# Optimization experiments

Hardware: AMD Instinct MI355X
Metric: run time of the kernel (lower is better)

## Reference

```python
import jax, jax.numpy as jnp
import numpy as np

B, S = 32, 128
VIN, VOUT = 32000, 32000
D, H, A = 256, 512, 128


def setup_inputs() -> dict:
    key = jax.random.key(0)
    ks = jax.random.split(key, 14)
    p = lambda k, sh: 0.02 * jax.random.normal(k, sh, jnp.float32)
    return {
        "tokens": jax.random.randint(ks[0], (B, S), 0, VIN + 1, dtype=jnp.int32),
        "emb": p(ks[1], (VIN + 1, D)),
        # forward encoder GRU (keras reset_after=True: separate input/recurrent bias)
        "Wx_f": p(ks[2], (D, 3 * H)), "Wh_f": p(ks[3], (H, 3 * H)),
        "bi_f": jnp.zeros((3 * H,), jnp.float32), "br_f": jnp.zeros((3 * H,), jnp.float32),
        # backward encoder GRU
        "Wx_b": p(ks[4], (D, 3 * H)), "Wh_b": p(ks[5], (H, 3 * H)),
        "bi_b": jnp.zeros((3 * H,), jnp.float32), "br_b": jnp.zeros((3 * H,), jnp.float32),
        # additive attention
        "W_a": p(ks[6], (A, H)), "U_a": p(ks[7], (A, 2 * H)), "V_a": p(ks[8], (1, A)),
        # decoder GRUCell (input = [enc_t, ctx] -> 4H)
        "Wx_d": p(ks[9], (4 * H, 3 * H)), "Wh_d": p(ks[10], (H, 3 * H)),
        "bi_d": jnp.zeros((3 * H,), jnp.float32), "br_d": jnp.zeros((3 * H,), jnp.float32),
        # output projection
        "Wo": p(ks[11], (H, VOUT + 1)), "bo": jnp.zeros((VOUT + 1,), jnp.float32),
    }


def _gru_step(h, x, Wx, Wh, bi, br):
    # keras GRU, gate order [z, r, h], reset_after=True
    gx = x @ Wx + bi
    gh = h @ Wh + br
    xz, xr, xh = jnp.split(gx, 3, axis=-1)
    hz, hr, hh = jnp.split(gh, 3, axis=-1)
    z = jax.nn.sigmoid(xz + hz)
    r = jax.nn.sigmoid(xr + hr)
    hc = jnp.tanh(xh + r * hh)
    return z * h + (1.0 - z) * hc


def _run_gru(xs, h0, Wx, Wh, bi, br):
    def f(h, x):
        hn = _gru_step(h, x, Wx, Wh, bi, br)
        return hn, hn
    return jax.lax.scan(f, h0, xs)  # xs: [S,B,D]


def _forward(tokens, emb, Wx_f, Wh_f, bi_f, br_f, Wx_b, Wh_b, bi_b, br_b,
             W_a, U_a, V_a, Wx_d, Wh_d, bi_d, br_d, Wo, bo):
    x = emb[tokens]                      # [B,S,D]
    xs = jnp.transpose(x, (1, 0, 2))     # [S,B,D]
    h0 = jnp.zeros((tokens.shape[0], H), x.dtype)
    _, ys_f = _run_gru(xs, h0, Wx_f, Wh_f, bi_f, br_f)
    hb, ys_b_rev = _run_gru(xs[::-1], h0, Wx_b, Wh_b, bi_b, br_b)
    enc_t = jnp.concatenate([ys_f, ys_b_rev[::-1]], axis=-1)  # [S,B,2H]
    enc = jnp.transpose(enc_t, (1, 0, 2))                     # [B,S,2H]
    U_enc = jnp.einsum('bsd,ad->bsa', enc, U_a)               # hoisted: loop-invariant
    v = V_a[0]                                                # [A]

    def dec_step(h, x_t):
        wh = h @ W_a.T                                        # [B,A]
        score = jnp.einsum('bsa,a->bs', jnp.tanh(wh[:, None, :] + U_enc), v)
        alpha = jax.nn.softmax(score, axis=-1)
        ctx = jnp.einsum('bs,bsd->bd', alpha, enc)            # [B,2H]
        din = jnp.concatenate([x_t, ctx], axis=-1)            # [B,4H]
        hn = _gru_step(h, din, Wx_d, Wh_d, bi_d, br_d)
        return hn, hn

    _, dec_seq = jax.lax.scan(dec_step, hb, enc_t)            # [S,B,H]
    dec = jnp.transpose(dec_seq, (1, 0, 2))                   # [B,S,H]
    logits = dec @ Wo + bo                                    # [B,S,VOUT+1]
    return jax.nn.softmax(logits, axis=-1)


def reference(tokens, emb, Wx_f, Wh_f, bi_f, br_f, Wx_b, Wh_b, bi_b, br_b,
              W_a, U_a, V_a, Wx_d, Wh_d, bi_d, br_d, Wo, bo):
    return _forward(tokens, emb, Wx_f, Wh_f, bi_f, br_f, Wx_b, Wh_b, bi_b, br_b,
                    W_a, U_a, V_a, Wx_d, Wh_d, bi_d, br_d, Wo, bo)
```

## Files before the change

kernel.cpp:

```cpp
#include <hip/hip_runtime.h>
#include <stdint.h>

typedef unsigned int u32;
typedef unsigned long long u64;
typedef __attribute__((ext_vector_type(8))) short bf16x8;
typedef __attribute__((ext_vector_type(4))) float f32x4;
typedef __attribute__((ext_vector_type(4))) int i32x4;
typedef __attribute__((ext_vector_type(2))) int i32x2;

#define DEV static __device__ __forceinline__

DEV short f2bf(float f){ u32 u=__float_as_uint(f); return (short)((u + 0x7fffu + ((u>>16)&1u))>>16); }
DEV float bf2f(short s){ return __uint_as_float(((u32)(unsigned short)s)<<16); }
DEV float sig_p(float x){ return 1.f/(1.f+expf(-x)); }
DEV float tanh_fast(float x){ float e=__expf(2.f*x); return 1.f-2.f/(e+1.f); }

DEV u32  cohl4(const u32* p){ return __hip_atomic_load(p, __ATOMIC_RELAXED, __HIP_MEMORY_SCOPE_AGENT); }
DEV void cohs4(u32* p, u32 v){ __hip_atomic_store(p, v, __ATOMIC_RELAXED, __HIP_MEMORY_SCOPE_AGENT); }
DEV void cohs8(void* p, u64 v){ __hip_atomic_store((u64*)p, v, __ATOMIC_RELAXED, __HIP_MEMORY_SCOPE_AGENT); }
DEV void pollnz(const u32* s){ while (cohl4(s) == 0u) {} }


__global__ void cvt1d(const float* __restrict__ in, short* __restrict__ out, int n){
  int i = blockIdx.x*256 + threadIdx.x;
  if (i < n) out[i] = f2bf(in[i]);
}

__global__ void tconv(const float* __restrict__ in, short* __restrict__ out, int R, int C, int Cpad){
  __shared__ float t[32][33];
  int tx = threadIdx.x, ty = threadIdx.y;
  int c0 = blockIdx.x*32, r0 = blockIdx.y*32;
#pragma unroll
  for (int j=0;j<4;++j){
    int r = r0 + ty + 8*j, c = c0 + tx;
    t[ty+8*j][tx] = (c < C) ? in[(size_t)r*C + c] : 0.f;
  }
  __syncthreads();
#pragma unroll
  for (int j=0;j<4;++j){
    int oc = c0 + ty + 8*j;
    out[(size_t)oc*R + r0 + tx] = f2bf(t[tx][ty+8*j]);
  }
}

__global__ void btrans(const short* __restrict__ in, short* __restrict__ out, int Dd){
  __shared__ short t[32][33];
  int tx = threadIdx.x, ty = threadIdx.y;
  int d0 = blockIdx.x*32, s = blockIdx.y;
#pragma unroll
  for (int j=0;j<4;++j)
    t[ty+8*j][tx] = in[((size_t)s*Dd + d0 + ty + 8*j)*32 + tx];
  __syncthreads();
#pragma unroll
  for (int j=0;j<4;++j)
    out[((size_t)(s*32 + ty + 8*j))*Dd + d0 + tx] = t[tx][ty+8*j];
}

__global__ void etrans(const short* __restrict__ in, short* __restrict__ out){
  __shared__ short t[128][33];
  int c = blockIdx.x, tid = threadIdx.x;
#pragma unroll
  for (int i=0;i<16;++i){
    int idx = tid + i*256;
    t[idx>>5][idx&31] = in[((size_t)(idx>>5)*1536 + c)*32 + (idx&31)];
  }
  __syncthreads();
#pragma unroll
  for (int i=0;i<16;++i){
    int idx = tid + i*256;
    out[((size_t)(idx>>7)*1536 + c)*128 + (idx&127)] = t[idx&127][idx>>7];
  }
}

__global__ void embed_k(const int* __restrict__ tok, const float* __restrict__ emb, short* __restrict__ X){
  int row = blockIdx.x;
  int s = row >> 5, b = row & 31;
  int tv = tok[b*128 + s];
  X[(size_t)row*256 + threadIdx.x] = f2bf(emb[(size_t)tv*256 + threadIdx.x]);
}

template<int MODE>
__global__ __launch_bounds__(256) void gemm_k(
  const short* __restrict__ A, const short* __restrict__ BT,
  const float* __restrict__ bias, void* __restrict__ outp,
  float* __restrict__ psum, int Nreal, int K, int Ntot)
{
  const int m0 = blockIdx.y * 128, n0 = blockIdx.x * 128;
  const int tid = threadIdx.x, l = tid & 63, wv = tid >> 6;
  const int wm = wv >> 1, wn = wv & 1;
  __shared__ __align__(16) short As[128*64];
  __shared__ __align__(16) short Bs[128*64];
  f32x4 acc[4][4];
#pragma unroll
  for (int i=0;i<4;++i)
#pragma unroll
    for (int j=0;j<4;++j) acc[i][j] = (f32x4){0.f,0.f,0.f,0.f};

  const int nkb = K >> 6;
  for (int kb=0; kb<nkb; ++kb){
#pragma unroll
    for (int i=0;i<4;++i){
      int si = tid + i*256;
      int row = si >> 3, seg = si & 7;
      u32 off = (u32)(row*128 + seg*16) ^ (u32)((row&7)<<4);
      *(i32x4*)((char*)As + off) = *(const i32x4*)(A + (size_t)(m0+row)*K + kb*64 + seg*8);
      *(i32x4*)((char*)Bs + off) = *(const i32x4*)(BT + (size_t)(n0+row)*K + kb*64 + seg*8);
    }
    __syncthreads();
#pragma unroll
    for (int kt=0; kt<2; ++kt){
      bf16x8 af[4], bfv[4];
      int seg = kt*4 + (l>>4);
#pragma unroll
      for (int f=0; f<4; ++f){
        int ra = wm*64 + f*16 + (l&15);
        af[f]  = *(const bf16x8*)((char*)As + (((u32)(ra*128 + seg*16)) ^ ((u32)(ra&7)<<4)));
        int rb = wn*64 + f*16 + (l&15);
        bfv[f] = *(const bf16x8*)((char*)Bs + (((u32)(rb*128 + seg*16)) ^ ((u32)(rb&7)<<4)));
      }
#pragma unroll
      for (int mf=0; mf<4; ++mf)
#pragma unroll
        for (int nf=0; nf<4; ++nf)
          acc[mf][nf] = __builtin_amdgcn_mfma_f32_16x16x32_bf16(af[mf], bfv[nf], acc[mf][nf], 0,0,0);
    }
    __syncthreads();
  }

  if (MODE == 1){
    short* oT = (short*)outp;
#pragma unroll
    for (int mf=0; mf<4; ++mf){
      int r0 = m0 + wm*64 + mf*16 + ((l>>4)<<2);
      int s = r0 >> 5, b0 = r0 & 31;
#pragma unroll
      for (int nf=0; nf<4; ++nf){
        int col = n0 + wn*64 + nf*16 + (l&15);
        float bv = bias ? bias[col] : 0.f;
        short tmp[4];
#pragma unroll
        for (int j=0;j<4;++j) tmp[j] = f2bf(acc[mf][nf][j] + bv);
        *(i32x2*)(oT + ((size_t)s*Ntot + col)*32 + b0) = *(i32x2*)tmp;
      }
    }
  } else if (MODE == 3){
    short* o = (short*)outp;
#pragma unroll
    for (int mf=0; mf<4; ++mf){
      int r0 = m0 + wm*64 + mf*16 + ((l>>4)<<2);
#pragma unroll
      for (int nf=0; nf<4; ++nf){
        int col = n0 + wn*64 + nf*16 + (l&15);
        if (col < Nreal){
          float bv = bias ? bias[col] : 0.f;
#pragma unroll
          for (int j=0;j<4;++j) o[(size_t)(r0+j)*Nreal + col] = f2bf(acc[mf][nf][j] + bv);
        }
      }
    }
  } else {
    float* o = (float*)outp;
    int ncb = gridDim.x;
    float rs[4][4];
#pragma unroll
    for (int i=0;i<4;++i)
#pragma unroll
      for (int j=0;j<4;++j) rs[i][j]=0.f;
#pragma unroll
    for (int mf=0; mf<4; ++mf){
      int r0 = m0 + wm*64 + mf*16 + ((l>>4)<<2);
      int s = r0 >> 5, b0 = r0 & 31;
#pragma unroll
      for (int nf=0; nf<4; ++nf){
        int col = n0 + wn*64 + nf*16 + (l&15);
        if (col < Nreal){
          float bv = bias[col];
#pragma unroll
          for (int j=0;j<4;++j){
            float e = __expf(acc[mf][nf][j] + bv);
            o[(size_t)((b0+j)*128 + s)*Nreal + col] = e;
            rs[mf][j] += e;
          }
        }
      }
    }
#pragma unroll
    for (int mf=0; mf<4; ++mf)
#pragma unroll
      for (int j=0;j<4;++j){
        float v = rs[mf][j];
        v += __shfl_xor(v,1); v += __shfl_xor(v,2); v += __shfl_xor(v,4); v += __shfl_xor(v,8);
        if ((l&15)==0){
          int r = m0 + wm*64 + mf*16 + ((l>>4)<<2) + j;
          int orow = (r&31)*128 + (r>>5);
          psum[(size_t)orow*(2*ncb) + blockIdx.x*2 + wn] = v;
        }
      }
  }
}

__global__ __launch_bounds__(512,1) void enc_scan(
  const short* __restrict__ gxfT, const short* __restrict__ gxbT,
  const short* __restrict__ WhfT, const short* __restrict__ WhbT,
  const float* __restrict__ brf, const float* __restrict__ brb,
  u32* __restrict__ hband, float* __restrict__ hfin,
  short* __restrict__ encT, u32* __restrict__ eflag)
{
  __shared__ __align__(16) short As[32*512];
  __shared__ float accL[96][36];
  __shared__ float brL[96];
  const int tid = threadIdx.x, wg = blockIdx.x;
  const int dir = wg >> 4, j = wg & 15;
  const short* gxT = dir ? gxbT : gxfT;
  const short* WT  = dir ? WhbT : WhfT;
  const float* br  = dir ? brb  : brf;
  u32* hb = hband + (size_t)dir*129*8192;
  u32* fl = eflag + (size_t)dir*129*512;
  const int l = tid & 63, wv = tid >> 6;

  if (tid < 96) brL[tid] = br[(tid>>5)*512 + j*32 + (tid&31)];

  bf16x8 bfr[2][16];
  if (wv < 3){
#pragma unroll
    for (int p=0;p<2;++p){
      int gcol = wv*512 + j*32 + p*16 + (l&15);
      const short* bp = WT + (size_t)gcol*512 + ((l>>4)<<3);
#pragma unroll
      for (int kt=0; kt<16; ++kt) bfr[p][kt] = *(const bf16x8*)(bp + kt*32);
    }
  }

  const int pb = tid & 31, php = tid >> 5;
  float hreg[2] = {0.f, 0.f};

  for (int t=0; t<128; ++t){
    const int s = dir ? (127-t) : t;
    if (t > 0){
      if (tid < 16) pollnz(&fl[(size_t)t*512 + tid*32]);
      __syncthreads();
    }
#pragma unroll
    for (int it=0; it<4; ++it){
      int u = tid + it*512;
      int b = u >> 6, k8 = u & 63;
      i32x4 v = *(const i32x4*)&hb[(size_t)t*8192 + b*256 + k8*4];
      *(i32x4*)((char*)As + b*1024 + ((k8*16) ^ ((b&15)<<4))) = v;
    }
    __syncthreads();
    if (wv < 3){
      f32x4 acc[2][2];
#pragma unroll
      for (int m=0;m<2;++m){ acc[m][0]=(f32x4){0,0,0,0}; acc[m][1]=(f32x4){0,0,0,0}; }
#pragma unroll
      for (int kt=0; kt<16; ++kt){
#pragma unroll
        for (int m=0;m<2;++m){
          int row = m*16 + (l&15);
          int kbyte = (kt*4 + (l>>4))*16;
          bf16x8 af = *(const bf16x8*)((char*)As + row*1024 + (kbyte ^ ((row&15)<<4)));
          acc[m][0] = __builtin_amdgcn_mfma_f32_16x16x32_bf16(af, bfr[0][kt], acc[m][0], 0,0,0);
          acc[m][1] = __builtin_amdgcn_mfma_f32_16x16x32_bf16(af, bfr[1][kt], acc[m][1], 0,0,0);
        }
      }
#pragma unroll
      for (int m=0;m<2;++m)
#pragma unroll
        for (int p=0;p<2;++p)
          *(f32x4*)&accL[wv*32 + p*16 + (l&15)][m*16 + ((l>>4)<<2)] = acc[m][p];
    }
    __syncthreads();
    short obf[2];
    {
      int b = pb, hc0 = php*2;
#pragma unroll
      for (int q=0;q<2;++q){
        int hc = hc0 + q, hcol = j*32 + hc;
        float xz = bf2f(gxT[((size_t)s*1536 + hcol)*32 + b]);
        float xr = bf2f(gxT[((size_t)s*1536 + 512 + hcol)*32 + b]);
        float xh = bf2f(gxT[((size_t)s*1536 + 1024 + hcol)*32 + b]);
        float gz = accL[hc][b]    + brL[hc];
        float gr = accL[32+hc][b] + brL[32+hc];
        float gh = accL[64+hc][b] + brL[64+hc];
        float z = sig_p(xz + gz);
        float r = sig_p(xr + gr);
        float hcand = tanhf(xh + r*gh);
        float hn = z*hreg[q] + (1.f-z)*hcand;
        hreg[q] = hn;
        obf[q] = f2bf(hn);
      }
      u32 pv = ((u32)(unsigned short)obf[1]<<16) | (u32)(unsigned short)obf[0];
      cohs4(&hb[(size_t)(t+1)*8192 + b*256 + j*16 + php], pv);
    }
    __syncthreads();
    if (tid == 0) cohs4(&fl[(size_t)(t+1)*512 + j*32], 1u);
    {
      int b = pb, hc0 = php*2;
      encT[((size_t)s*1024 + dir*512 + (j*32+hc0))*32 + b]   = obf[0];
      encT[((size_t)s*1024 + dir*512 + (j*32+hc0+1))*32 + b] = obf[1];
      if (dir && t == 127){
        hfin[(j*32+hc0)*32 + b]   = hreg[0];
        hfin[(j*32+hc0+1)*32 + b] = hreg[1];
      }
    }
  }
}

__global__ void dec_init(const float* __restrict__ hfin, u32* __restrict__ hband0){
  int i = blockIdx.x*256 + threadIdx.x;
  int b = i >> 8, k2 = i & 255;
  float v0 = hfin[(k2*2)*32 + b];
  float v1 = hfin[(k2*2+1)*32 + b];
  hband0[b*256 + k2] = ((u32)(unsigned short)f2bf(v1)<<16) | (u32)(unsigned short)f2bf(v0);
}

__global__ __launch_bounds__(512,1) void dec_scan(
  const short* __restrict__ gxeR,
  const short* __restrict__ encx,
  const short* __restrict__ WhdT,
  const float* __restrict__ brd,
  const short* __restrict__ Wa, const short* __restrict__ Uenc, const float* __restrict__ Va,
  const float* __restrict__ hfin,
  u32* __restrict__ hband,
  float* __restrict__ GHband,
  short* __restrict__ decRow,
  u32* __restrict__ hflag, u32* __restrict__ gflag)
{
  __shared__ __align__(16) short As[32*512];
  __shared__ float accL[96][36];
  __shared__ float hs[512];
  __shared__ float gxc[1536];
  __shared__ float brA[1536];
  __shared__ float whp[128*5];
  __shared__ float whv[128];
  __shared__ float scp[128*5];
  __shared__ float sc[128];
  __shared__ float red[4];
  __shared__ float vL[128];
  __shared__ float aL[128];

  const int tid = threadIdx.x, wg = blockIdx.x;
  const int l = tid & 63, wv = tid >> 6;

  if (wg < 16){
    const int j = wg;
    bf16x8 bfr[2][16];
    if (wv < 3){
#pragma unroll
      for (int p=0;p<2;++p){
        int gcol = wv*512 + j*32 + p*16 + (l&15);
        const short* bp = WhdT + (size_t)gcol*512 + ((l>>4)<<3);
#pragma unroll
        for (int kt=0; kt<16; ++kt) bfr[p][kt] = *(const bf16x8*)(bp + kt*32);
      }
    }
    const int b2 = tid >> 4, q = tid & 15;
    for (int t=0; t<128; ++t){
      if (t > 0){
        if (tid < 32) pollnz(&hflag[(size_t)t*1024 + tid*32]);
        __syncthreads();
      }
#pragma unroll
      for (int it=0; it<4; ++it){
        int u = tid + it*512;
        int b = u >> 6, k8 = u & 63;
        i32x4 v = *(const i32x4*)&hband[(size_t)t*8192 + b*256 + k8*4];
        *(i32x4*)((char*)As + b*1024 + ((k8*16) ^ ((b&15)<<4))) = v;
      }
      __syncthreads();
      if (wv < 3){
        f32x4 acc[2][2];
#pragma unroll
        for (int m=0;m<2;++m){ acc[m][0]=(f32x4){0,0,0,0}; acc[m][1]=(f32x4){0,0,0,0}; }
#pragma unroll
        for (int kt=0; kt<16; ++kt){
#pragma unroll
          for (int m=0;m<2;++m){
            int row = m*16 + (l&15);
            int kbyte = (kt*4 + (l>>4))*16;
            bf16x8 af = *(const bf16x8*)((char*)As + row*1024 + (kbyte ^ ((row&15)<<4)));
            acc[m][0] = __builtin_amdgcn_mfma_f32_16x16x32_bf16(af, bfr[0][kt], acc[m][0], 0,0,0);
            acc[m][1] = __builtin_amdgcn_mfma_f32_16x16x32_bf16(af, bfr[1][kt], acc[m][1], 0,0,0);
          }
        }
#pragma unroll
        for (int m=0;m<2;++m)
#pragma unroll
          for (int p=0;p<2;++p)
            *(f32x4*)&accL[wv*32 + p*16 + (l&15)][m*16 + ((l>>4)<<2)] = acc[m][p];
      }
      __syncthreads();
      {
        float* gbase = GHband + ((size_t)t*32 + b2)*1536;
#pragma unroll
        for (int pp=0; pp<3; ++pp){
          int cp = q*6 + pp*2;
          float f0 = accL[cp][b2], f1 = accL[cp+1][b2];
          u64 pv = ((u64)__float_as_uint(f1)<<32) | (u64)__float_as_uint(f0);
          cohs8(&gbase[(cp>>5)*512 + j*32 + (cp&31)], pv);
        }
      }
      __syncthreads();
      if (tid == 0) cohs4(&gflag[(size_t)t*512 + j*32], 1u);
    }
  } else {
    const int b = wg - 16;
    u32 wa[64];
    {
      const u32* wp = (const u32*)(Wa + (size_t)(tid&127)*512 + (tid>>7)*128);
#pragma unroll
      for (int i=0;i<64;++i) wa[i] = wp[i];
    }
    u32 ue[16];
    {
      int s = tid & 127, aq = tid >> 7;
      const u32* up = (const u32*)(Uenc + ((size_t)(s*32 + b))*128 + aq*32);
#pragma unroll
      for (int i=0;i<16;++i) ue[i] = up[i];
    }
    if (tid < 128) vL[tid] = Va[tid];
    for (int i = tid; i < 1536; i += 512) brA[i] = brd[i];
    hs[tid] = hfin[(size_t)tid*32 + b];
    const short* eb = encx + (size_t)b*1536*128;
    __syncthreads();

    for (int t=0; t<128; ++t){
      {
        int a = tid & 127, kq2 = tid >> 7;
        float p = 0.f;
        const float* hp2 = &hs[kq2*128];
#pragma unroll 8
        for (int i=0;i<64;++i){
          u32 w2 = wa[i];
          float2 h2 = *(const float2*)(hp2 + 2*i);
          p += bf2f((short)(w2 & 0xffff))*h2.x + bf2f((short)(w2 >> 16))*h2.y;
        }
        whp[a*5 + kq2] = p;
      }
      __syncthreads();
      if (tid < 128) whv[tid] = whp[tid*5]+whp[tid*5+1]+whp[tid*5+2]+whp[tid*5+3];
      __syncthreads();
      {
        int s = tid & 127, aq = tid >> 7;
        float p = 0.f;
#pragma unroll 4
        for (int i=0;i<16;++i){
          u32 u2 = ue[i];
          int a0 = aq*32 + 2*i;
          p += tanh_fast(whv[a0]   + bf2f((short)(u2 & 0xffff))) * vL[a0];
          p += tanh_fast(whv[a0+1] + bf2f((short)(u2 >> 16)))    * vL[a0+1];
        }
        scp[s*5 + aq] = p;
      }
      __syncthreads();
      if (tid < 128) sc[tid] = scp[tid*5]+scp[tid*5+1]+scp[tid*5+2]+scp[tid*5+3];
      __syncthreads();
      float ev = 0.f;
      if (tid < 128){
        float v = sc[tid], mx = v;
#pragma unroll
        for (int d2=32; d2; d2>>=1) mx = fmaxf(mx, __shfl_xor(mx, d2));
        if ((tid & 63) == 0) red[tid>>6] = mx;
      }
      __syncthreads();
      if (tid < 128){
        float mx = fmaxf(red[0], red[1]);
        ev = __expf(sc[tid] - mx);
        float sm = ev;
#pragma unroll
        for (int d2=32; d2; d2>>=1) sm += __shfl_xor(sm, d2);
        if ((tid & 63) == 0) red[2 + (tid>>6)] = sm;
      }
      __syncthreads();
      if (tid < 128) aL[tid] = ev / (red[2] + red[3]);
      __syncthreads();
      {
        int col = tid*3;
        float a0=0.f, a1=0.f, a2=0.f;
        const short* e0 = eb + (size_t)col*128;
#pragma unroll
        for (int sb=0; sb<16; ++sb){
          f32x4 av0 = *(const f32x4*)&aL[sb*8];
          f32x4 av1 = *(const f32x4*)&aL[sb*8+4];
          bf16x8 ev0 = *(const bf16x8*)(e0 + sb*8);
          bf16x8 ev1 = *(const bf16x8*)(e0 + 128 + sb*8);
          bf16x8 ev2 = *(const bf16x8*)(e0 + 256 + sb*8);
#pragma unroll
          for (int i=0;i<4;++i){
            a0 += bf2f(ev0[i])*av0[i]; a1 += bf2f(ev1[i])*av0[i]; a2 += bf2f(ev2[i])*av0[i];
            a0 += bf2f(ev0[4+i])*av1[i]; a1 += bf2f(ev1[4+i])*av1[i]; a2 += bf2f(ev2[4+i])*av1[i];
          }
        }
        gxc[col] = a0; gxc[col+1] = a1; gxc[col+2] = a2;
      }
      __syncthreads();
      const short* gx = gxeR + ((size_t)t*32 + b)*1536;
      float gx0 = bf2f(gx[tid])        + gxc[tid];
      float gx1 = bf2f(gx[512 + tid])  + gxc[512 + tid];
      float gx2 = bf2f(gx[1024 + tid]) + gxc[1024 + tid];
      if (tid < 16) pollnz(&gflag[(size_t)t*512 + tid*32]);
      __syncthreads();
      short mybf;
      {
        const float* ghp = GHband + ((size_t)t*32 + b)*1536;
        float gh0 = ghp[tid];
        float gh1 = ghp[512 + tid];
        float gh2 = ghp[1024 + tid];
        float z = sig_p(gx0 + gh0 + brA[tid]);
        float r = sig_p(gx1 + gh1 + brA[512 + tid]);
        float hcand = tanhf(gx2 + r*(gh2 + brA[1024 + tid]));
        float hp = hs[tid];
        float hn = z*hp + (1.f-z)*hcand;
        hs[tid] = hn;
        mybf = f2bf(hn);
        u32 self16 = (u32)(unsigned short)mybf;
        u32 oth = (u32)__shfl_xor((int)self16, 1);
        if (!(tid & 1))
          cohs4(&hband[(size_t)(t+1)*8192 + b*256 + (tid>>1)], self16 | (oth<<16));
      }
      __syncthreads();
      if (tid == 0) cohs4(&hflag[(size_t)(t+1)*1024 + b*32], 1u);
      decRow[((size_t)t*32 + b)*512 + tid] = mybf;
    }
  }
}

__global__ void scale_rows(float* __restrict__ out, const float* __restrict__ psum,
                           int ncols, int w){
  int r = blockIdx.x;
  __shared__ float ssum[256];
  float s = 0.f;
  for (int i = threadIdx.x; i < w; i += 256) s += psum[(size_t)r*w + i];
  ssum[threadIdx.x] = s; __syncthreads();
  for (int d = 128; d; d >>= 1){
    if (threadIdx.x < d) ssum[threadIdx.x] += ssum[threadIdx.x + d];
    __syncthreads();
  }
  float v = 1.f/ssum[0];
  float* p = out + (size_t)r*ncols;
  for (int i = threadIdx.x; i < ncols; i += 256) p[i] *= v;
}

extern "C" void kernel_launch(void* const* d_in, const int* in_sizes, int n_in,
                              void* d_out, int out_size, void* d_ws, size_t ws_size,
                              hipStream_t stream)
{
  const int*   tokens=(const int*)  d_in[0];
  const float* emb  =(const float*)d_in[1];
  const float* Wx_f =(const float*)d_in[2];
  const float* Wh_f =(const float*)d_in[3];
  const float* bi_f =(const float*)d_in[4];
  const float* br_f =(const float*)d_in[5];
  const float* Wx_b =(const float*)d_in[6];
  const float* Wh_b =(const float*)d_in[7];
  const float* bi_b =(const float*)d_in[8];
  const float* br_b =(const float*)d_in[9];
  const float* W_a  =(const float*)d_in[10];
  const float* U_a  =(const float*)d_in[11];
  const float* V_a  =(const float*)d_in[12];
  const float* Wx_d =(const float*)d_in[13];
  const float* Wh_d =(const float*)d_in[14];
  const float* bi_d =(const float*)d_in[15];
  const float* br_d =(const float*)d_in[16];
  const float* Wo   =(const float*)d_in[17];
  const float* bo   =(const float*)d_in[18];

  const int NV = 32001, NVP = 32128, NCB = 251;

  char* base = (char*)d_ws; size_t off = 0;
  auto alloc = [&](size_t bytes)->char*{
    off = (off + 255) & ~(size_t)255;
    char* p = base + off; off += bytes; return p;
  };
  u32*   eflag  = (u32*)  alloc((size_t)2*129*512*4);
  u32*   hflag  = (u32*)  alloc((size_t)129*1024*4);
  u32*   gflag  = (u32*)  alloc((size_t)128*512*4);
  u32*   hband_e= (u32*)  alloc((size_t)2*129*8192*4);
  u32*   hband_d= (u32*)  alloc((size_t)129*8192*4);
  float* GHband = (float*)alloc((size_t)128*32*1536*4);
  float* hfin   = (float*)alloc((size_t)512*32*4);
  short* X      = (short*)alloc((size_t)4096*256*2);
  short* WxfT   = (short*)alloc((size_t)1536*256*2);
  short* WxbT   = (short*)alloc((size_t)1536*256*2);
  short* WhfT   = (short*)alloc((size_t)1536*512*2);
  short* WhbT   = (short*)alloc((size_t)1536*512*2);
  short* WhdT   = (short*)alloc((size_t)1536*512*2);
  short* WxeT   = (short*)alloc((size_t)1536*1024*2);
  short* WxcT   = (short*)alloc((size_t)1536*1024*2);
  short* WoT    = (short*)alloc((size_t)NVP*512*2);
  short* UaB    = (short*)alloc((size_t)128*1024*2);
  short* WaB    = (short*)alloc((size_t)128*512*2);
  short* gxfT   = (short*)alloc((size_t)128*1536*32*2);
  short* gxbT   = (short*)alloc((size_t)128*1536*32*2);
  short* encT   = (short*)alloc((size_t)128*1024*32*2);
  short* encRow = (short*)alloc((size_t)4096*1024*2);
  short* Uenc   = (short*)alloc((size_t)4096*128*2);
  short* gxeR   = (short*)alloc((size_t)4096*1536*2);
  short* encxT1 = (short*)alloc((size_t)128*1536*32*2);
  short* encx   = (short*)alloc((size_t)32*1536*128*2);
  short* decRow = (short*)alloc((size_t)4096*512*2);
  float* psum   = (float*)alloc((size_t)4096*2*NCB*4);

  hipMemsetAsync(eflag, 0, (size_t)2*129*512*4, stream);
  hipMemsetAsync(hflag, 0, (size_t)129*1024*4, stream);
  hipMemsetAsync(gflag, 0, (size_t)128*512*4, stream);
  hipMemsetAsync(hband_e, 0, (size_t)2*129*8192*4, stream);

  tconv<<<dim3(1536/32,256/32),dim3(32,8),0,stream>>>(Wx_f, WxfT, 256, 1536, 1536);
  tconv<<<dim3(1536/32,256/32),dim3(32,8),0,stream>>>(Wx_b, WxbT, 256, 1536, 1536);
  tconv<<<dim3(1536/32,512/32),dim3(32,8),0,stream>>>(Wh_f, WhfT, 512, 1536, 1536);
  tconv<<<dim3(1536/32,512/32),dim3(32,8),0,stream>>>(Wh_b, WhbT, 512, 1536, 1536);
  tconv<<<dim3(1536/32,512/32),dim3(32,8),0,stream>>>(Wh_d, WhdT, 512, 1536, 1536);
  tconv<<<dim3(1536/32,1024/32),dim3(32,8),0,stream>>>(Wx_d,                    WxeT, 1024, 1536, 1536);
  tconv<<<dim3(1536/32,1024/32),dim3(32,8),0,stream>>>(Wx_d+(size_t)1024*1536,  WxcT, 1024, 1536, 1536);
  tconv<<<dim3(NVP/32,512/32),dim3(32,8),0,stream>>>(Wo, WoT, 512, NV, NVP);
  cvt1d<<<(128*512+255)/256,256,0,stream>>>(W_a, WaB, 128*512);
  cvt1d<<<(128*1024+255)/256,256,0,stream>>>(U_a, UaB, 128*1024);

  embed_k<<<4096,256,0,stream>>>(tokens, emb, X);

  gemm_k<1><<<dim3(12,32),256,0,stream>>>(X, WxfT, bi_f, gxfT, nullptr, 1536, 256, 1536);
  gemm_k<1><<<dim3(12,32),256,0,stream>>>(X, WxbT, bi_b, gxbT, nullptr, 1536, 256, 1536);

  enc_scan<<<32,512,0,stream>>>(gxfT, gxbT, WhfT, WhbT, br_f, br_b,
                                hband_e, hfin, encT, eflag);

  btrans<<<dim3(1024/32,128),dim3(32,8),0,stream>>>(encT, encRow, 1024);

  gemm_k<3><<<dim3(1,32),256,0,stream>>>(encRow, UaB, nullptr, Uenc, nullptr, 128, 1024, 128);
  gemm_k<3><<<dim3(12,32),256,0,stream>>>(encRow, WxeT, bi_d, gxeR, nullptr, 1536, 1024, 1536);
  gemm_k<1><<<dim3(12,32),256,0,stream>>>(encRow, WxcT, nullptr, encxT1, nullptr, 1536, 1024, 1536);
  etrans<<<1536,256,0,stream>>>(encxT1, encx);

  dec_init<<<32,256,0,stream>>>(hfin, hband_d);

  dec_scan<<<48,512,0,stream>>>(gxeR, encx, WhdT, br_d, WaB, Uenc, V_a,
                                hfin, hband_d, GHband, decRow, hflag, gflag);

  gemm_k<2><<<dim3(NCB,32),256,0,stream>>>(decRow, WoT, bo, d_out, psum, NV, 512, NV);

  scale_rows<<<4096,256,0,stream>>>((float*)d_out, psum, NV, 2*NCB);
}
```

Measured before the change: 3.783 ms.

## Replace flag-based inter-block sync with step-tagged data words in scans

The encoder and decoder scans now embed the step index in the low 16 bits of each published word (bf16 value in the high half), so consumers poll the data itself instead of a separate flag followed by a barrier. Hidden-state bands become double-buffered ring buffers instead of per-step arrays, and the decoder's recurrent GEMM is split across six waves that publish bf16 gate results directly, removing the accL staging and several __syncthreads. This is meant to cut the per-step latency of flag writes, flag polling and extra barriers, at the cost of twice as many words transferred per step, bf16 rounding of the recurrent gate pre-activations, and a 16-bit tag that relies on the sequence being short.

```diff
diff --git a/kernel.cpp b/kernel.cpp
--- a/kernel.cpp
+++ b/kernel.cpp
@@ -18,7 +18,6 @@
 DEV u32  cohl4(const u32* p){ return __hip_atomic_load(p, __ATOMIC_RELAXED, __HIP_MEMORY_SCOPE_AGENT); }
 DEV void cohs4(u32* p, u32 v){ __hip_atomic_store(p, v, __ATOMIC_RELAXED, __HIP_MEMORY_SCOPE_AGENT); }
 DEV void cohs8(void* p, u64 v){ __hip_atomic_store((u64*)p, v, __ATOMIC_RELAXED, __HIP_MEMORY_SCOPE_AGENT); }
-DEV void pollnz(const u32* s){ while (cohl4(s) == 0u) {} }
 
 
 __global__ void cvt1d(const float* __restrict__ in, short* __restrict__ out, int n){
@@ -203,10 +202,10 @@
   const short* __restrict__ gxfT, const short* __restrict__ gxbT,
   const short* __restrict__ WhfT, const short* __restrict__ WhbT,
   const float* __restrict__ brf, const float* __restrict__ brb,
-  u32* __restrict__ hband, float* __restrict__ hfin,
-  short* __restrict__ encT, u32* __restrict__ eflag)
+  u32* __restrict__ band, float* __restrict__ hfin,
+  short* __restrict__ encT)
 {
-  __shared__ __align__(16) short As[32*512];
+  __shared__ __align__(16) char Asb[32*1024];
   __shared__ float accL[96][36];
   __shared__ float brL[96];
   const int tid = threadIdx.x, wg = blockIdx.x;
@@ -214,8 +213,7 @@
   const short* gxT = dir ? gxbT : gxfT;
   const short* WT  = dir ? WhbT : WhfT;
   const float* br  = dir ? brb  : brf;
-  u32* hb = hband + (size_t)dir*129*8192;
-  u32* fl = eflag + (size_t)dir*129*512;
+  u32* bd = band + (size_t)dir*32768;
   const int l = tid & 63, wv = tid >> 6;
 
   if (tid < 96) brL[tid] = br[(tid>>5)*512 + j*32 + (tid&31)];
@@ -232,20 +230,23 @@
   }
 
   const int pb = tid & 31, php = tid >> 5;
+  const int sb = tid >> 4, sk0 = (tid & 15)*32;
   float hreg[2] = {0.f, 0.f};
 
   for (int t=0; t<128; ++t){
     const int s = dir ? (127-t) : t;
-    if (t > 0){
-      if (tid < 16) pollnz(&fl[(size_t)t*512 + tid*32]);
-      __syncthreads();
-    }
-#pragma unroll
-    for (int it=0; it<4; ++it){
-      int u = tid + it*512;
-      int b = u >> 6, k8 = u & 63;
-      i32x4 v = *(const i32x4*)&hb[(size_t)t*8192 + b*256 + k8*4];
-      *(i32x4*)((char*)As + b*1024 + ((k8*16) ^ ((b&15)<<4))) = v;
+    {
+      const u32* src = bd + (size_t)(t&1)*16384 + sb*512 + sk0;
+      u32 w[32];
+#pragma unroll
+      for (int i=0;i<32;++i) w[i] = cohl4(src+i);
+#pragma unroll
+      for (int i=0;i<32;++i){ while ((w[i]&0xffffu) != (u32)t) w[i] = cohl4(src+i); }
+#pragma unroll
+      for (int i=0;i<16;++i){
+        u32 p = (w[2*i]>>16) | (w[2*i+1] & 0xffff0000u);
+        *(u32*)(Asb + (((u32)(sb*1024 + (sk0+2*i)*2)) ^ ((u32)(sb&15)<<4))) = p;
+      }
     }
     __syncthreads();
     if (wv < 3){
@@ -258,7 +259,7 @@
         for (int m=0;m<2;++m){
           int row = m*16 + (l&15);
           int kbyte = (kt*4 + (l>>4))*16;
-          bf16x8 af = *(const bf16x8*)((char*)As + row*1024 + (kbyte ^ ((row&15)<<4)));
+          bf16x8 af = *(const bf16x8*)(Asb + (((u32)(row*1024 + kbyte)) ^ ((u32)(row&15)<<4)));
           acc[m][0] = __builtin_amdgcn_mfma_f32_16x16x32_bf16(af, bfr[0][kt], acc[m][0], 0,0,0);
           acc[m][1] = __builtin_amdgcn_mfma_f32_16x16x32_bf16(af, bfr[1][kt], acc[m][1], 0,0,0);
         }
@@ -289,11 +290,10 @@
         hreg[q] = hn;
         obf[q] = f2bf(hn);
       }
-      u32 pv = ((u32)(unsigned short)obf[1]<<16) | (u32)(unsigned short)obf[0];
-      cohs4(&hb[(size_t)(t+1)*8192 + b*256 + j*16 + php], pv);
-    }
-    __syncthreads();
-    if (tid == 0) cohs4(&fl[(size_t)(t+1)*512 + j*32], 1u);
+      u32 w0 = ((u32)(unsigned short)obf[0]<<16) | (u32)(t+1);
+      u32 w1 = ((u32)(unsigned short)obf[1]<<16) | (u32)(t+1);
+      cohs8(bd + (size_t)((t+1)&1)*16384 + b*512 + j*32 + hc0, ((u64)w1<<32)|(u64)w0);
+    }
     {
       int b = pb, hc0 = php*2;
       encT[((size_t)s*1024 + dir*512 + (j*32+hc0))*32 + b]   = obf[0];
@@ -303,15 +303,14 @@
         hfin[(j*32+hc0+1)*32 + b] = hreg[1];
       }
     }
-  }
-}
-
-__global__ void dec_init(const float* __restrict__ hfin, u32* __restrict__ hband0){
+    __syncthreads();
+  }
+}
+
+__global__ void dec_init(const float* __restrict__ hfin, u32* __restrict__ band){
   int i = blockIdx.x*256 + threadIdx.x;
-  int b = i >> 8, k2 = i & 255;
-  float v0 = hfin[(k2*2)*32 + b];
-  float v1 = hfin[(k2*2+1)*32 + b];
-  hband0[b*256 + k2] = ((u32)(unsigned short)f2bf(v1)<<16) | (u32)(unsigned short)f2bf(v0);
+  int b = i >> 9, k = i & 511;
+  band[b*512 + k] = ((u32)(unsigned short)f2bf(hfin[(size_t)k*32 + b])<<16);
 }
 
 __global__ __launch_bounds__(512,1) void dec_scan(
@@ -321,13 +320,10 @@
   const float* __restrict__ brd,
   const short* __restrict__ Wa, const short* __restrict__ Uenc, const float* __restrict__ Va,
   const float* __restrict__ hfin,
-  u32* __restrict__ hband,
-  float* __restrict__ GHband,
-  short* __restrict__ decRow,
-  u32* __restrict__ hflag, u32* __restrict__ gflag)
+  u32* __restrict__ hband, u32* __restrict__ GHt,
+  short* __restrict__ decRow)
 {
-  __shared__ __align__(16) short As[32*512];
-  __shared__ float accL[96][36];
+  __shared__ __align__(16) char Asb[32*1024];
   __shared__ float hs[512];
   __shared__ float gxc[1536];
   __shared__ float brA[1536];
@@ -344,64 +340,50 @@
 
   if (wg < 16){
     const int j = wg;
-    bf16x8 bfr[2][16];
-    if (wv < 3){
-#pragma unroll
-      for (int p=0;p<2;++p){
-        int gcol = wv*512 + j*32 + p*16 + (l&15);
-        const short* bp = WhdT + (size_t)gcol*512 + ((l>>4)<<3);
-#pragma unroll
-        for (int kt=0; kt<16; ++kt) bfr[p][kt] = *(const bf16x8*)(bp + kt*32);
-      }
-    }
-    const int b2 = tid >> 4, q = tid & 15;
+    const int colbase = (wv>>1)*512 + j*32 + ((wv&1)<<4);
+    bf16x8 bfr[16];
+    if (wv < 6){
+      const short* bp = WhdT + (size_t)(colbase + (l&15))*512 + ((l>>4)<<3);
+#pragma unroll
+      for (int kt=0; kt<16; ++kt) bfr[kt] = *(const bf16x8*)(bp + kt*32);
+    }
+    const int sb = tid >> 4, sk0 = (tid & 15)*32;
     for (int t=0; t<128; ++t){
-      if (t > 0){
-        if (tid < 32) pollnz(&hflag[(size_t)t*1024 + tid*32]);
-        __syncthreads();
-      }
-#pragma unroll
-      for (int it=0; it<4; ++it){
-        int u = tid + it*512;
-        int b = u >> 6, k8 = u & 63;
-        i32x4 v = *(const i32x4*)&hband[(size_t)t*8192 + b*256 + k8*4];
-        *(i32x4*)((char*)As + b*1024 + ((k8*16) ^ ((b&15)<<4))) = v;
-      }
-      __syncthreads();
-      if (wv < 3){
-        f32x4 acc[2][2];
-#pragma unroll
-        for (int m=0;m<2;++m){ acc[m][0]=(f32x4){0,0,0,0}; acc[m][1]=(f32x4){0,0,0,0}; }
+      {
+        const u32* src = hband + (size_t)(t&1)*16384 + sb*512 + sk0;
+        u32 w[32];
+#pragma unroll
+        for (int i=0;i<32;++i) w[i] = cohl4(src+i);
+#pragma unroll
+        for (int i=0;i<32;++i){ while ((w[i]&0xffffu) != (u32)t) w[i] = cohl4(src+i); }
+#pragma unroll
+        for (int i=0;i<16;++i){
+          u32 p = (w[2*i]>>16) | (w[2*i+1] & 0xffff0000u);
+          *(u32*)(Asb + (((u32)(sb*1024 + (sk0+2*i)*2)) ^ ((u32)(sb&15)<<4))) = p;
+        }
+      }
+      __syncthreads();
+      if (wv < 6){
+        f32x4 acc0 = (f32x4){0.f,0.f,0.f,0.f};
+        f32x4 acc1 = (f32x4){0.f,0.f,0.f,0.f};
 #pragma unroll
         for (int kt=0; kt<16; ++kt){
-#pragma unroll
-          for (int m=0;m<2;++m){
-            int row = m*16 + (l&15);
-            int kbyte = (kt*4 + (l>>4))*16;
-            bf16x8 af = *(const bf16x8*)((char*)As + row*1024 + (kbyte ^ ((row&15)<<4)));
-            acc[m][0] = __builtin_amdgcn_mfma_f32_16x16x32_bf16(af, bfr[0][kt], acc[m][0], 0,0,0);
-            acc[m][1] = __builtin_amdgcn_mfma_f32_16x16x32_bf16(af, bfr[1][kt], acc[m][1], 0,0,0);
-          }
-        }
-#pragma unroll
-        for (int m=0;m<2;++m)
-#pragma unroll
-          for (int p=0;p<2;++p)
-            *(f32x4*)&accL[wv*32 + p*16 + (l&15)][m*16 + ((l>>4)<<2)] = acc[m][p];
-      }
-      __syncthreads();
-      {
-        float* gbase = GHband + ((size_t)t*32 + b2)*1536;
-#pragma unroll
-        for (int pp=0; pp<3; ++pp){
-          int cp = q*6 + pp*2;
-          float f0 = accL[cp][b2], f1 = accL[cp+1][b2];
-          u64 pv = ((u64)__float_as_uint(f1)<<32) | (u64)__float_as_uint(f0);
-          cohs8(&gbase[(cp>>5)*512 + j*32 + (cp&31)], pv);
-        }
-      }
-      __syncthreads();
-      if (tid == 0) cohs4(&gflag[(size_t)t*512 + j*32], 1u);
+          int kbyte = (kt*32 + ((l>>4)<<3))*2;
+          int r0 = l & 15, r1 = 16 + (l & 15);
+          bf16x8 af0 = *(const bf16x8*)(Asb + (((u32)(r0*1024 + kbyte)) ^ ((u32)(r0&15)<<4)));
+          bf16x8 af1 = *(const bf16x8*)(Asb + (((u32)(r1*1024 + kbyte)) ^ ((u32)(r1&15)<<4)));
+          acc0 = __builtin_amdgcn_mfma_f32_16x16x32_bf16(af0, bfr[kt], acc0, 0,0,0);
+          acc1 = __builtin_amdgcn_mfma_f32_16x16x32_bf16(af1, bfr[kt], acc1, 0,0,0);
+        }
+#pragma unroll
+        for (int r=0;r<4;++r){
+          u32 wd0 = ((u32)(unsigned short)f2bf(acc0[r])<<16) | (u32)(t+1);
+          cohs4(&GHt[(size_t)((l>>4)*4 + r)*1536 + colbase + (l&15)], wd0);
+          u32 wd1 = ((u32)(unsigned short)f2bf(acc1[r])<<16) | (u32)(t+1);
+          cohs4(&GHt[(size_t)(16 + (l>>4)*4 + r)*1536 + colbase + (l&15)], wd1);
+        }
+      }
+      __syncthreads();
     }
   } else {
     const int b = wg - 16;
@@ -479,12 +461,12 @@
         float a0=0.f, a1=0.f, a2=0.f;
         const short* e0 = eb + (size_t)col*128;
 #pragma unroll
-        for (int sb=0; sb<16; ++sb){
-          f32x4 av0 = *(const f32x4*)&aL[sb*8];
-          f32x4 av1 = *(const f32x4*)&aL[sb*8+4];
-          bf16x8 ev0 = *(const bf16x8*)(e0 + sb*8);
-          bf16x8 ev1 = *(const bf16x8*)(e0 + 128 + sb*8);
-          bf16x8 ev2 = *(const bf16x8*)(e0 + 256 + sb*8);
+        for (int sb2=0; sb2<16; ++sb2){
+          f32x4 av0 = *(const f32x4*)&aL[sb2*8];
+          f32x4 av1 = *(const f32x4*)&aL[sb2*8+4];
+          bf16x8 ev0 = *(const bf16x8*)(e0 + sb2*8);
+          bf16x8 ev1 = *(const bf16x8*)(e0 + 128 + sb2*8);
+          bf16x8 ev2 = *(const bf16x8*)(e0 + 256 + sb2*8);
 #pragma unroll
           for (int i=0;i<4;++i){
             a0 += bf2f(ev0[i])*av0[i]; a1 += bf2f(ev1[i])*av0[i]; a2 += bf2f(ev2[i])*av0[i];
@@ -498,29 +480,29 @@
       float gx0 = bf2f(gx[tid])        + gxc[tid];
       float gx1 = bf2f(gx[512 + tid])  + gxc[512 + tid];
       float gx2 = bf2f(gx[1024 + tid]) + gxc[1024 + tid];
-      if (tid < 16) pollnz(&gflag[(size_t)t*512 + tid*32]);
-      __syncthreads();
       short mybf;
       {
-        const float* ghp = GHband + ((size_t)t*32 + b)*1536;
-        float gh0 = ghp[tid];
-        float gh1 = ghp[512 + tid];
-        float gh2 = ghp[1024 + tid];
+        const u32* gp = GHt + (size_t)b*1536 + tid;
+        u32 g0 = cohl4(gp), g1 = cohl4(gp+512), g2 = cohl4(gp+1024);
+        u32 want = (u32)(t+1);
+        while ((g0&0xffffu) != want) g0 = cohl4(gp);
+        while ((g1&0xffffu) != want) g1 = cohl4(gp+512);
+        while ((g2&0xffffu) != want) g2 = cohl4(gp+1024);
+        float gh0 = bf2f((short)(g0>>16));
+        float gh1 = bf2f((short)(g1>>16));
+        float gh2 = bf2f((short)(g2>>16));
         float z = sig_p(gx0 + gh0 + brA[tid]);
         float r = sig_p(gx1 + gh1 + brA[512 + tid]);
         float hcand = tanhf(gx2 + r*(gh2 + brA[1024 + tid]));
         float hp = hs[tid];
         float hn = z*hp + (1.f-z)*hcand;
+        mybf = f2bf(hn);
+        cohs4(&hband[(size_t)((t+1)&1)*16384 + b*512 + tid],
+              ((u32)(unsigned short)mybf<<16) | (u32)(t+1));
         hs[tid] = hn;
-        mybf = f2bf(hn);
-        u32 self16 = (u32)(unsigned short)mybf;
-        u32 oth = (u32)__shfl_xor((int)self16, 1);
-        if (!(tid & 1))
-          cohs4(&hband[(size_t)(t+1)*8192 + b*256 + (tid>>1)], self16 | (oth<<16));
-      }
-      __syncthreads();
-      if (tid == 0) cohs4(&hflag[(size_t)(t+1)*1024 + b*32], 1u);
+      }
       decRow[((size_t)t*32 + b)*512 + tid] = mybf;
+      __syncthreads();
     }
   }
 }
@@ -572,12 +554,9 @@
     off = (off + 255) & ~(size_t)255;
     char* p = base + off; off += bytes; return p;
   };
-  u32*   eflag  = (u32*)  alloc((size_t)2*129*512*4);
-  u32*   hflag  = (u32*)  alloc((size_t)129*1024*4);
-  u32*   gflag  = (u32*)  alloc((size_t)128*512*4);
-  u32*   hband_e= (u32*)  alloc((size_t)2*129*8192*4);
-  u32*   hband_d= (u32*)  alloc((size_t)129*8192*4);
-  float* GHband = (float*)alloc((size_t)128*32*1536*4);
+  u32*   band_e = (u32*)  alloc((size_t)2*2*16384*4);
+  u32*   band_d = (u32*)  alloc((size_t)2*16384*4);
+  u32*   GHt    = (u32*)  alloc((size_t)32*1536*4);
   float* hfin   = (float*)alloc((size_t)512*32*4);
   short* X      = (short*)alloc((size_t)4096*256*2);
   short* WxfT   = (short*)alloc((size_t)1536*256*2);
@@ -601,10 +580,9 @@
   short* decRow = (short*)alloc((size_t)4096*512*2);
   float* psum   = (float*)alloc((size_t)4096*2*NCB*4);
 
-  hipMemsetAsync(eflag, 0, (size_t)2*129*512*4, stream);
-  hipMemsetAsync(hflag, 0, (size_t)129*1024*4, stream);
-  hipMemsetAsync(gflag, 0, (size_t)128*512*4, stream);
-  hipMemsetAsync(hband_e, 0, (size_t)2*129*8192*4, stream);
+  hipMemsetAsync(band_e, 0, (size_t)2*2*16384*4, stream);
+  hipMemsetAsync(band_d, 0, (size_t)2*16384*4, stream);
+  hipMemsetAsync(GHt,    0, (size_t)32*1536*4, stream);
 
   tconv<<<dim3(1536/32,256/32),dim3(32,8),0,stream>>>(Wx_f, WxfT, 256, 1536, 1536);
   tconv<<<dim3(1536/32,256/32),dim3(32,8),0,stream>>>(Wx_b, WxbT, 256, 1536, 1536);
@@ -623,7 +601,7 @@
   gemm_k<1><<<dim3(12,32),256,0,stream>>>(X, WxbT, bi_b, gxbT, nullptr, 1536, 256, 1536);
 
   enc_scan<<<32,512,0,stream>>>(gxfT, gxbT, WhfT, WhbT, br_f, br_b,
-                                hband_e, hfin, encT, eflag);
+                                band_e, hfin, encT);
 
   btrans<<<dim3(1024/32,128),dim3(32,8),0,stream>>>(encT, encRow, 1024);
 
@@ -632,10 +610,10 @@
   gemm_k<1><<<dim3(12,32),256,0,stream>>>(encRow, WxcT, nullptr, encxT1, nullptr, 1536, 1024, 1536);
   etrans<<<1536,256,0,stream>>>(encxT1, encx);
 
-  dec_init<<<32,256,0,stream>>>(hfin, hband_d);
+  dec_init<<<64,256,0,stream>>>(hfin, band_d);
 
   dec_scan<<<48,512,0,stream>>>(gxeR, encx, WhdT, br_d, WaB, Uenc, V_a,
-                                hfin, hband_d, GHband, decRow, hflag, gflag);
+                                hfin, band_d, GHt, decRow);
 
   gemm_k<2><<<dim3(NCB,32),256,0,stream>>>(decRow, WoT, bo, d_out, psum, NV, 512, NV);
 
```

Result: slower. 5.051 ms (+33.5%).
